# Optimization experiments

Hardware: AMD Instinct MI355X
Metric: run time of the kernel (lower is better)

The kernel has to match this reference:

```python
import jax, jax.numpy as jnp
import numpy as np

GROUP_SIZE = 128
ZERO_POINT = 8  # 4-bit symmetric zero point


def setup_inputs() -> dict:
    key = jax.random.key(0)
    k1, k2, k3, k4, k5, k6 = jax.random.split(key, 6)
    B, S, IN, OUT, RANK = 4, 2048, 4096, 4096, 32
    n_groups = IN // GROUP_SIZE  # 32
    x = jax.random.normal(k1, (B, S, IN), dtype=jnp.float32)
    q = jax.random.randint(k2, (OUT, IN), 0, 16, dtype=jnp.int32)  # 4-bit codes
    scales = jax.random.uniform(k3, (OUT, n_groups), dtype=jnp.float32)
    U = jax.random.normal(k4, (OUT, RANK), dtype=jnp.float32)
    V = jax.random.normal(k5, (RANK, IN), dtype=jnp.float32)
    bias = jax.random.normal(k6, (OUT,), dtype=jnp.float32)
    return {"x": x, "q": q, "scales": scales, "U": U, "V": V, "bias": bias}


def reference(x, q, scales, U, V, bias):
    out_f, in_f = q.shape
    n_groups = scales.shape[1]
    # Dequantize: per-group scaled 4-bit codes -> [out, in]
    qf = (q.astype(scales.dtype) - ZERO_POINT).reshape(out_f, n_groups, GROUP_SIZE)
    W = (qf * scales[:, :, None]).reshape(out_f, in_f)
    # Low-rank correction
    W = W + U @ V
    # F.linear: y = x @ W^T + b
    return jnp.einsum("bsi,oi->bso", x, W) + bias
```

## Files before the change

### kernel.cpp

```cpp
#include <hip/hip_runtime.h>
#include <hip/hip_bf16.h>

#define GAS __attribute__((address_space(1)))
#define LAS __attribute__((address_space(3)))

typedef __bf16 bf16x8 __attribute__((ext_vector_type(8)));
typedef float f32x16 __attribute__((ext_vector_type(16)));

constexpr int Kd = 4096;
constexpr int Nd = 4096;
constexpr int RANKd = 32;
constexpr int NG = 32;
constexpr int BM = 128, BN = 128, BK = 64;

constexpr int BWR = 32, BWC = 256;
constexpr int NBUILD = (Nd / BWR) * (Kd / BWC);

__global__ __launch_bounds__(256) void prep(
    const int* __restrict__ q, const float* __restrict__ scales,
    const float* __restrict__ U, const float* __restrict__ V,
    __hip_bfloat16* __restrict__ W,
    const float* __restrict__ x, __hip_bfloat16* __restrict__ xb)
{
  __shared__ float V_s[RANKd][BWC + 4];
  __shared__ float U_s[BWR][RANKd + 1];

  const int t = threadIdx.x;
  const int bid = blockIdx.x;

  if (bid >= NBUILD) {
    const size_t base = (size_t)(bid - NBUILD) * 8192;
    #pragma unroll
    for (int i = 0; i < 4; ++i) {
      const size_t idx = base + i * 2048 + t * 8;
      float4 a = *(const float4*)(x + idx);
      float4 b = *(const float4*)(x + idx + 4);
      union { __hip_bfloat16 h[8]; int4 v; } u;
      u.h[0] = __float2bfloat16(a.x); u.h[1] = __float2bfloat16(a.y);
      u.h[2] = __float2bfloat16(a.z); u.h[3] = __float2bfloat16(a.w);
      u.h[4] = __float2bfloat16(b.x); u.h[5] = __float2bfloat16(b.y);
      u.h[6] = __float2bfloat16(b.z); u.h[7] = __float2bfloat16(b.w);
      *(int4*)(xb + idx) = u.v;
    }
    return;
  }

  const int bx = bid & 15;
  const int by = bid >> 4;
  const int n0 = by * BWR;
  const int k0 = bx * BWC;

  {
    const int idx = t * 4;
    const int row = idx >> 5, rr = idx & 31;
    float4 uv = *(const float4*)(U + (size_t)(n0 + row) * RANKd + rr);
    U_s[row][rr] = uv.x; U_s[row][rr + 1] = uv.y;
    U_s[row][rr + 2] = uv.z; U_s[row][rr + 3] = uv.w;
  }
  #pragma unroll
  for (int i = 0; i < 8; ++i) {
    const int idx = i * 1024 + t * 4;
    const int vr = idx >> 8, vc = idx & 255;
    *(float4*)&V_s[vr][vc] = *(const float4*)(V + (size_t)vr * Kd + k0 + vc);
  }
  __syncthreads();

  const int rs = t >> 5;
  const int cs = t & 31;
  const int row0 = n0 + rs * 4;
  const int c0 = cs * 4;
  const int c1 = 128 + cs * 4;
  const int g0 = k0 >> 7, g1 = g0 + 1;

  float acc[4][8];
  #pragma unroll
  for (int j = 0; j < 4; ++j) {
    const int* qr = q + (size_t)(row0 + j) * Kd + k0;
    int4 a = *(const int4*)(qr + c0);
    int4 b = *(const int4*)(qr + c1);
    const float s0 = scales[(size_t)(row0 + j) * NG + g0];
    const float s1 = scales[(size_t)(row0 + j) * NG + g1];
    acc[j][0] = (float)(a.x - 8) * s0; acc[j][1] = (float)(a.y - 8) * s0;
    acc[j][2] = (float)(a.z - 8) * s0; acc[j][3] = (float)(a.w - 8) * s0;
    acc[j][4] = (float)(b.x - 8) * s1; acc[j][5] = (float)(b.y - 8) * s1;
    acc[j][6] = (float)(b.z - 8) * s1; acc[j][7] = (float)(b.w - 8) * s1;
  }

  #pragma unroll 4
  for (int r = 0; r < RANKd; ++r) {
    float4 v0 = *(const float4*)&V_s[r][c0];
    float4 v1 = *(const float4*)&V_s[r][c1];
    #pragma unroll
    for (int j = 0; j < 4; ++j) {
      const float u = U_s[rs * 4 + j][r];
      acc[j][0] += u * v0.x; acc[j][1] += u * v0.y;
      acc[j][2] += u * v0.z; acc[j][3] += u * v0.w;
      acc[j][4] += u * v1.x; acc[j][5] += u * v1.y;
      acc[j][6] += u * v1.z; acc[j][7] += u * v1.w;
    }
  }

  #pragma unroll
  for (int j = 0; j < 4; ++j) {
    union { __hip_bfloat16 h[4]; uint2 v; } o0, o1;
    o0.h[0] = __float2bfloat16(acc[j][0]); o0.h[1] = __float2bfloat16(acc[j][1]);
    o0.h[2] = __float2bfloat16(acc[j][2]); o0.h[3] = __float2bfloat16(acc[j][3]);
    o1.h[0] = __float2bfloat16(acc[j][4]); o1.h[1] = __float2bfloat16(acc[j][5]);
    o1.h[2] = __float2bfloat16(acc[j][6]); o1.h[3] = __float2bfloat16(acc[j][7]);
    __hip_bfloat16* wr = W + (size_t)(row0 + j) * Kd + k0;
    *(uint2*)(wr + c0) = o0.v;
    *(uint2*)(wr + c1) = o1.v;
  }
}

#define WAIT_VM6 asm volatile("s_waitcnt vmcnt(6)" ::: "memory")
#define WAIT_VM0 asm volatile("s_waitcnt vmcnt(0)" ::: "memory")
#define WAIT_NONE ((void)0)

#define ISSUE6(H, SLOT)                                                         \
  {                                                                             \
    char* sb_ = smc + (SLOT) * 24576;                                           \
    const size_t ko_ = (size_t)(H) * 32;                                        \
    __builtin_amdgcn_global_load_lds((GAS void*)(ag0 + ko_),                    \
        (LAS void*)(sb_ + ldsA), 16, 0, 0);                                     \
    __builtin_amdgcn_global_load_lds((GAS void*)(ag0 + 16 * Kd + ko_),          \
        (LAS void*)(sb_ + ldsA + 1024), 16, 0, 0);                              \
    __builtin_amdgcn_global_load_lds((GAS void*)(bg0 + ko_),                    \
        (LAS void*)(sb_ + ldsB), 16, 0, 0);                                     \
    __builtin_amdgcn_global_load_lds((GAS void*)(bg0 + 16 * Kd + ko_),          \
        (LAS void*)(sb_ + ldsB + 1024), 16, 0, 0);                              \
    __builtin_amdgcn_global_load_lds((GAS void*)(bg0 + 32 * Kd + ko_),          \
        (LAS void*)(sb_ + ldsB + 2048), 16, 0, 0);                              \
    __builtin_amdgcn_global_load_lds((GAS void*)(bg0 + 48 * Kd + ko_),          \
        (LAS void*)(sb_ + ldsB + 3072), 16, 0, 0);                              \
  }

#define GPHASE(G, SCUR, SNXT2, WAITSTMT, DO_ISSUE)                              \
  {                                                                             \
    const char* as_ = (const char*)smc + (SCUR) * 24576;                        \
    bf16x8 af0[4], af1[4], bfA[2], bfB[2];                                      \
    _Pragma("unroll")                                                           \
    for (int mi = 0; mi < 4; ++mi) {                                            \
      af0[mi] = *(const bf16x8*)(as_ + aro + mi * 2048 + cq0);                  \
      af1[mi] = *(const bf16x8*)(as_ + aro + mi * 2048 + cq1);                  \
    }                                                                           \
    _Pragma("unroll")                                                           \
    for (int nj = 0; nj < 2; ++nj) {                                            \
      bfA[nj] = *(const bf16x8*)(as_ + bro + nj * 2048 + cq0);                  \
      bfB[nj] = *(const bf16x8*)(as_ + bro + nj * 2048 + cq1);                  \
    }                                                                           \
    __builtin_amdgcn_sched_barrier(0);                                          \
    if (DO_ISSUE) { ISSUE6((G) + 2, SNXT2); }                                   \
    __builtin_amdgcn_sched_barrier(0);                                          \
    WAITSTMT;                                                                   \
    __builtin_amdgcn_s_barrier();                                               \
    asm volatile("s_waitcnt lgkmcnt(0)" ::: "memory");                          \
    __builtin_amdgcn_sched_barrier(0);                                          \
    __builtin_amdgcn_s_setprio(1);                                              \
    _Pragma("unroll")                                                           \
    for (int mi = 0; mi < 4; ++mi)                                              \
      _Pragma("unroll")                                                         \
      for (int nj = 0; nj < 2; ++nj)                                            \
        acc[mi][nj] = __builtin_amdgcn_mfma_f32_32x32x16_bf16(                  \
            af0[mi], bfA[nj], acc[mi][nj], 0, 0, 0);                            \
    _Pragma("unroll")                                                           \
    for (int mi = 0; mi < 4; ++mi)                                              \
      _Pragma("unroll")                                                         \
      for (int nj = 0; nj < 2; ++nj)                                            \
        acc[mi][nj] = __builtin_amdgcn_mfma_f32_32x32x16_bf16(                  \
            af1[mi], bfB[nj], acc[mi][nj], 0, 0, 0);                            \
    __builtin_amdgcn_s_setprio(0);                                              \
    __builtin_amdgcn_s_barrier();                                               \
  }

__global__ __launch_bounds__(256, 2) void gemm128(
    const __hip_bfloat16* __restrict__ A, const __hip_bfloat16* __restrict__ Bt,
    const float* __restrict__ bias, float* __restrict__ C)
{
  __shared__ __align__(16) char sm[73728];
  char* const smc = sm;

  int bx, by;
  {
    const int bid = blockIdx.x;
    if (gridDim.x == 1024) {
      const int x = bid & 7, loc = bid >> 3;
      by = x * 8 + (loc & 7);
      bx = loc >> 3;
    } else {
      by = bid >> 4;
      bx = bid & 15;
    }
  }
  const int bm0 = by * 128, bn0 = bx * 256;

  const int t = threadIdx.x;
  const int l = t & 63, w = t >> 6;

  const int sr   = l >> 2;
  const int schk = (l & 3) ^ ((l >> 3) & 3);
  const __hip_bfloat16* ag0 = A  + (size_t)(bm0 + w * 32 + sr) * Kd + schk * 8;
  const __hip_bfloat16* bg0 = Bt + (size_t)(bn0 + w * 64 + sr) * Kd + schk * 8;
  const int ldsA = w * 2048 + l * 16;
  const int ldsB = 8192 + w * 4096 + l * 16;

  const int rl = l & 31, kh = l >> 5, swz = (rl >> 1) & 3;
  const int aro = rl * 64;
  const int bro = 8192 + (w * 64 + rl) * 64;
  const int cq0 = (kh ^ swz) * 16;
  const int cq1 = ((2 + kh) ^ swz) * 16;

  f32x16 acc[4][2];
  #pragma unroll
  for (int mi = 0; mi < 4; ++mi)
    #pragma unroll
    for (int nj = 0; nj < 2; ++nj)
      acc[mi][nj] = (f32x16)(0.f);

  ISSUE6(0, 0);
  ISSUE6(1, 1);
  WAIT_VM6;
  __builtin_amdgcn_s_barrier();
  __builtin_amdgcn_sched_barrier(0);

  for (int g = 0; g < 126; g += 3) {
    GPHASE(g,     0, 2, WAIT_VM6, 1);
    GPHASE(g + 1, 1, 0, WAIT_VM6, 1);
    GPHASE(g + 2, 2, 1, WAIT_VM6, 1);
  }
  GPHASE(126, 0, 2, WAIT_VM0, 0);
  GPHASE(127, 1, 0, WAIT_NONE, 0);

  #pragma unroll
  for (int nj = 0; nj < 2; ++nj) {
    const int col = bn0 + w * 64 + nj * 32 + rl;
    const float bz = bias[col];
    #pragma unroll
    for (int mi = 0; mi < 4; ++mi) {
      const int rbase = bm0 + mi * 32 + 4 * kh;
      #pragma unroll
      for (int reg = 0; reg < 16; ++reg) {
        const int row = rbase + (reg & 3) + 8 * (reg >> 2);
        C[(size_t)row * Nd + col] = acc[mi][nj][reg] + bz;
      }
    }
  }
}

#undef GPHASE
#undef ISSUE6

template <bool ABF16>
__global__ __launch_bounds__(256) void gemm_bt(
    const void* __restrict__ Ap, const __hip_bfloat16* __restrict__ Bt,
    const float* __restrict__ bias, float* __restrict__ C)
{
  __shared__ __hip_bfloat16 As[BM * BK];
  __shared__ __hip_bfloat16 Bs[BN * BK];

  const int t  = threadIdx.x;
  const int l  = t & 63;
  const int w  = t >> 6;
  const int wm = w >> 1;
  const int wn = w & 1;
  const int bm0 = blockIdx.y * BM;
  const int bn0 = blockIdx.x * BN;

  f32x16 acc[2][2];
  #pragma unroll
  for (int i = 0; i < 2; ++i)
    #pragma unroll
    for (int j = 0; j < 2; ++j)
      acc[i][j] = (f32x16)(0.f);

  const __hip_bfloat16* Abf = (const __hip_bfloat16*)Ap;
  const float*          A32 = (const float*)Ap;

  const int sr   = l >> 2;
  const int schk = (l & 3) ^ ((l >> 3) & 3);
  const __hip_bfloat16* ag0 = Abf + (size_t)(bm0 + w * 32 + sr) * Kd + schk * 8;
  const __hip_bfloat16* bg0 = Bt  + (size_t)(bn0 + w * 32 + sr) * Kd + schk * 8;
  char* asb = (char*)As + w * 2048;
  char* bsb = (char*)Bs + w * 2048;

  const int rl = l & 31, kh = l >> 5, swz = (rl >> 1) & 3;
  const char* Ard = (const char*)As + (wm * 64 + rl) * 64;
  const char* Brd = (const char*)Bs + (wn * 64 + rl) * 64;

  const int arow = t >> 1, aslab = t & 1, arx = (arow >> 1) & 3;
  const float* a32p = A32 + (size_t)(bm0 + arow) * Kd + aslab * 32;
  char* awr = (char*)As + aslab * 8192 + arow * 64;

  for (int kt = 0; kt < Kd / BK; ++kt) {
    if constexpr (ABF16) {
      const __hip_bfloat16* ag = ag0 + kt * BK;
      __builtin_amdgcn_global_load_lds((GAS void*)ag,               (LAS void*)asb,                16, 0, 0);
      __builtin_amdgcn_global_load_lds((GAS void*)(ag + 16 * Kd),   (LAS void*)(asb + 1024),       16, 0, 0);
      __builtin_amdgcn_global_load_lds((GAS void*)(ag + 32),        (LAS void*)(asb + 8192),       16, 0, 0);
      __builtin_amdgcn_global_load_lds((GAS void*)(ag + 16*Kd + 32),(LAS void*)(asb + 8192 + 1024),16, 0, 0);
    } else {
      const float* ap = a32p + kt * BK;
      #pragma unroll
      for (int cc = 0; cc < 4; ++cc) {
        float4 f0 = ((const float4*)ap)[cc * 2];
        float4 f1 = ((const float4*)ap)[cc * 2 + 1];
        union { __hip_bfloat16 h[8]; int4 v; } u;
        u.h[0] = __float2bfloat16(f0.x); u.h[1] = __float2bfloat16(f0.y);
        u.h[2] = __float2bfloat16(f0.z); u.h[3] = __float2bfloat16(f0.w);
        u.h[4] = __float2bfloat16(f1.x); u.h[5] = __float2bfloat16(f1.y);
        u.h[6] = __float2bfloat16(f1.z); u.h[7] = __float2bfloat16(f1.w);
        *(int4*)(awr + ((cc ^ arx) * 16)) = u.v;
      }
    }
    {
      const __hip_bfloat16* bg = bg0 + kt * BK;
      __builtin_amdgcn_global_load_lds((GAS void*)bg,               (LAS void*)bsb,                16, 0, 0);
      __builtin_amdgcn_global_load_lds((GAS void*)(bg + 16 * Kd),   (LAS void*)(bsb + 1024),       16, 0, 0);
      __builtin_amdgcn_global_load_lds((GAS void*)(bg + 32),        (LAS void*)(bsb + 8192),       16, 0, 0);
      __builtin_amdgcn_global_load_lds((GAS void*)(bg + 16*Kd + 32),(LAS void*)(bsb + 8192 + 1024),16, 0, 0);
    }

    __syncthreads();

    bf16x8 af[2][4], bfr[2][4];
    #pragma unroll
    for (int mi = 0; mi < 2; ++mi)
      #pragma unroll
      for (int ks = 0; ks < 4; ++ks)
        af[mi][ks] = *(const bf16x8*)(Ard + (ks >> 1) * 8192 + mi * 2048 +
                                      ((((ks & 1) * 2 + kh) ^ swz) * 16));
    #pragma unroll
    for (int nj = 0; nj < 2; ++nj)
      #pragma unroll
      for (int ks = 0; ks < 4; ++ks)
        bfr[nj][ks] = *(const bf16x8*)(Brd + (ks >> 1) * 8192 + nj * 2048 +
                                       ((((ks & 1) * 2 + kh) ^ swz) * 16));

    #pragma unroll
    for (int ks = 0; ks < 4; ++ks)
      #pragma unroll
      for (int mi = 0; mi < 2; ++mi)
        #pragma unroll
        for (int nj = 0; nj < 2; ++nj)
          acc[mi][nj] = __builtin_amdgcn_mfma_f32_32x32x16_bf16(
              af[mi][ks], bfr[nj][ks], acc[mi][nj], 0, 0, 0);

    __syncthreads();
  }

  #pragma unroll
  for (int nj = 0; nj < 2; ++nj) {
    const int col = bn0 + wn * 64 + nj * 32 + rl;
    const float bz = bias[col];
    #pragma unroll
    for (int mi = 0; mi < 2; ++mi) {
      const int rbase = bm0 + wm * 64 + mi * 32 + 4 * kh;
      #pragma unroll
      for (int reg = 0; reg < 16; ++reg) {
        const int row = rbase + (reg & 3) + 8 * (reg >> 2);
        C[(size_t)row * Nd + col] = acc[mi][nj][reg] + bz;
      }
    }
  }
}

extern "C" void kernel_launch(void* const* d_in, const int* in_sizes, int n_in,
                              void* d_out, int out_size, void* d_ws, size_t ws_size,
                              hipStream_t stream)
{
  const float* x      = (const float*)d_in[0];
  const int*   q      = (const int*)  d_in[1];
  const float* scales = (const float*)d_in[2];
  const float* U      = (const float*)d_in[3];
  const float* V      = (const float*)d_in[4];
  const float* bias   = (const float*)d_in[5];
  float* out = (float*)d_out;

  const int M = in_sizes[0] / Kd;

  __hip_bfloat16* Wb = (__hip_bfloat16*)d_ws;
  const size_t wbytes = (size_t)Nd * Kd * sizeof(__hip_bfloat16);
  const size_t xbytes = (size_t)M  * Kd * sizeof(__hip_bfloat16);

  if (ws_size >= wbytes + xbytes && (M % 128) == 0) {
    __hip_bfloat16* Xb = (__hip_bfloat16*)((char*)d_ws + wbytes);
    const int nconv = (int)(((size_t)M * Kd) / 8192);
    prep<<<dim3(NBUILD + nconv), dim3(256), 0, stream>>>(q, scales, U, V, Wb, x, Xb);
    const int nblk = (M / 128) * (Nd / 256);
    gemm128<<<dim3(nblk), dim3(256), 0, stream>>>(Xb, Wb, bias, out);
  } else {
    prep<<<dim3(NBUILD), dim3(256), 0, stream>>>(q, scales, U, V, Wb, x, nullptr);
    dim3 grid(Nd / BN, M / BM);
    gemm_bt<false><<<grid, dim3(256), 0, stream>>>((const void*)x, Wb, bias, out);
  }
}
```

Before: 551.9 us.

## Load GEMM A fragments directly from global into registers, staging only B in LDS

The 128x256 GEMM now reads its A operand fragments straight from global memory into registers, one phase ahead. Only the B tile is staged in LDS through the triple-buffered async global-to-LDS path. This shrinks LDS use from 72 KB to 48 KB, drops the trailing barrier in each phase, and rebalances the vmcnt waits. The cost is that all four waves fetch the same A rows, so A traffic through the cache grows fourfold. The A loads also arrive in un-swizzled per-lane order, which may cause uncoalesced access and longer load latency in the MFMA loop.

After: 854.5 us. +54.8%, slower.

```diff
diff --git a/kernel.cpp b/kernel.cpp
--- a/kernel.cpp
+++ b/kernel.cpp
@@ -113,18 +113,14 @@
   }
 }
 
-#define WAIT_VM6 asm volatile("s_waitcnt vmcnt(6)" ::: "memory")
-#define WAIT_VM0 asm volatile("s_waitcnt vmcnt(0)" ::: "memory")
-#define WAIT_NONE ((void)0)
-
-#define ISSUE6(H, SLOT)                                                         \
+#define WAIT_VM12 asm volatile("s_waitcnt vmcnt(12)" ::: "memory")
+#define WAIT_VM4  asm volatile("s_waitcnt vmcnt(4)"  ::: "memory")
+#define WAIT_VM0  asm volatile("s_waitcnt vmcnt(0)"  ::: "memory")
+
+#define ISSUE_B(H, SLOT)                                                        \
   {                                                                             \
-    char* sb_ = smc + (SLOT) * 24576;                                           \
+    char* sb_ = smc + (SLOT) * 16384;                                           \
     const size_t ko_ = (size_t)(H) * 32;                                        \
-    __builtin_amdgcn_global_load_lds((GAS void*)(ag0 + ko_),                    \
-        (LAS void*)(sb_ + ldsA), 16, 0, 0);                                     \
-    __builtin_amdgcn_global_load_lds((GAS void*)(ag0 + 16 * Kd + ko_),          \
-        (LAS void*)(sb_ + ldsA + 1024), 16, 0, 0);                              \
     __builtin_amdgcn_global_load_lds((GAS void*)(bg0 + ko_),                    \
         (LAS void*)(sb_ + ldsB), 16, 0, 0);                                     \
     __builtin_amdgcn_global_load_lds((GAS void*)(bg0 + 16 * Kd + ko_),          \
@@ -135,26 +131,22 @@
         (LAS void*)(sb_ + ldsB + 3072), 16, 0, 0);                              \
   }
 
-#define GPHASE(G, SCUR, SNXT2, WAITSTMT, DO_ISSUE)                              \
+#define GPHASE(G, SCUR, SNXT2, WAITSTMT, DO_ISSUE, DO_AF)                       \
   {                                                                             \
-    const char* as_ = (const char*)smc + (SCUR) * 24576;                        \
-    bf16x8 af0[4], af1[4], bfA[2], bfB[2];                                      \
-    _Pragma("unroll")                                                           \
-    for (int mi = 0; mi < 4; ++mi) {                                            \
-      af0[mi] = *(const bf16x8*)(as_ + aro + mi * 2048 + cq0);                  \
-      af1[mi] = *(const bf16x8*)(as_ + aro + mi * 2048 + cq1);                  \
-    }                                                                           \
+    const char* bs_ = (const char*)smc + (SCUR) * 16384;                        \
+    bf16x8 bfA[2], bfB[2];                                                      \
     _Pragma("unroll")                                                           \
     for (int nj = 0; nj < 2; ++nj) {                                            \
-      bfA[nj] = *(const bf16x8*)(as_ + bro + nj * 2048 + cq0);                  \
-      bfB[nj] = *(const bf16x8*)(as_ + bro + nj * 2048 + cq1);                  \
+      bfA[nj] = *(const bf16x8*)(bs_ + bro + nj * 2048 + cq0);                  \
+      bfB[nj] = *(const bf16x8*)(bs_ + bro + nj * 2048 + cq1);                  \
     }                                                                           \
     __builtin_amdgcn_sched_barrier(0);                                          \
-    if (DO_ISSUE) { ISSUE6((G) + 2, SNXT2); }                                   \
+    if (DO_ISSUE) { ISSUE_B((G) + 2, SNXT2); }                                  \
     __builtin_amdgcn_sched_barrier(0);                                          \
     WAITSTMT;                                                                   \
+    asm volatile("s_waitcnt lgkmcnt(0)" ::: "memory");                          \
+    __builtin_amdgcn_sched_barrier(0);                                          \
     __builtin_amdgcn_s_barrier();                                               \
-    asm volatile("s_waitcnt lgkmcnt(0)" ::: "memory");                          \
     __builtin_amdgcn_sched_barrier(0);                                          \
     __builtin_amdgcn_s_setprio(1);                                              \
     _Pragma("unroll")                                                           \
@@ -170,14 +162,23 @@
         acc[mi][nj] = __builtin_amdgcn_mfma_f32_32x32x16_bf16(                  \
             af1[mi], bfB[nj], acc[mi][nj], 0, 0, 0);                            \
     __builtin_amdgcn_s_setprio(0);                                              \
-    __builtin_amdgcn_s_barrier();                                               \
+    __builtin_amdgcn_sched_barrier(0);                                          \
+    if (DO_AF) {                                                                \
+      _Pragma("unroll")                                                         \
+      for (int mi = 0; mi < 4; ++mi) {                                          \
+        af0[mi] = *(const bf16x8*)(aP[mi]);                                     \
+        af1[mi] = *(const bf16x8*)(aP[mi] + 32);                                \
+        aP[mi] += 64;                                                           \
+      }                                                                         \
+    }                                                                           \
+    __builtin_amdgcn_sched_barrier(0);                                          \
   }
 
 __global__ __launch_bounds__(256, 2) void gemm128(
     const __hip_bfloat16* __restrict__ A, const __hip_bfloat16* __restrict__ Bt,
     const float* __restrict__ bias, float* __restrict__ C)
 {
-  __shared__ __align__(16) char sm[73728];
+  __shared__ __align__(16) char sm[49152];
   char* const smc = sm;
 
   int bx, by;
@@ -199,17 +200,19 @@
 
   const int sr   = l >> 2;
   const int schk = (l & 3) ^ ((l >> 3) & 3);
-  const __hip_bfloat16* ag0 = A  + (size_t)(bm0 + w * 32 + sr) * Kd + schk * 8;
   const __hip_bfloat16* bg0 = Bt + (size_t)(bn0 + w * 64 + sr) * Kd + schk * 8;
-  const int ldsA = w * 2048 + l * 16;
-  const int ldsB = 8192 + w * 4096 + l * 16;
+  const int ldsB = w * 4096 + l * 16;
 
   const int rl = l & 31, kh = l >> 5, swz = (rl >> 1) & 3;
-  const int aro = rl * 64;
-  const int bro = 8192 + (w * 64 + rl) * 64;
+  const int bro = (w * 64 + rl) * 64;
   const int cq0 = (kh ^ swz) * 16;
   const int cq1 = ((2 + kh) ^ swz) * 16;
 
+  const char* aP[4];
+  #pragma unroll
+  for (int mi = 0; mi < 4; ++mi)
+    aP[mi] = (const char*)(A + (size_t)(bm0 + mi * 32 + rl) * Kd) + kh * 16;
+
   f32x16 acc[4][2];
   #pragma unroll
   for (int mi = 0; mi < 4; ++mi)
@@ -217,19 +220,29 @@
     for (int nj = 0; nj < 2; ++nj)
       acc[mi][nj] = (f32x16)(0.f);
 
-  ISSUE6(0, 0);
-  ISSUE6(1, 1);
-  WAIT_VM6;
+  bf16x8 af0[4], af1[4];
+
+  ISSUE_B(0, 0);
+  ISSUE_B(1, 1);
+  __builtin_amdgcn_sched_barrier(0);
+  #pragma unroll
+  for (int mi = 0; mi < 4; ++mi) {
+    af0[mi] = *(const bf16x8*)(aP[mi]);
+    af1[mi] = *(const bf16x8*)(aP[mi] + 32);
+    aP[mi] += 64;
+  }
+  __builtin_amdgcn_sched_barrier(0);
+  WAIT_VM12;
   __builtin_amdgcn_s_barrier();
   __builtin_amdgcn_sched_barrier(0);
 
   for (int g = 0; g < 126; g += 3) {
-    GPHASE(g,     0, 2, WAIT_VM6, 1);
-    GPHASE(g + 1, 1, 0, WAIT_VM6, 1);
-    GPHASE(g + 2, 2, 1, WAIT_VM6, 1);
-  }
-  GPHASE(126, 0, 2, WAIT_VM0, 0);
-  GPHASE(127, 1, 0, WAIT_NONE, 0);
+    GPHASE(g,     0, 2, WAIT_VM4, 1, 1);
+    GPHASE(g + 1, 1, 0, WAIT_VM4, 1, 1);
+    GPHASE(g + 2, 2, 1, WAIT_VM4, 1, 1);
+  }
+  GPHASE(126, 0, 2, WAIT_VM0, 0, 1);
+  GPHASE(127, 1, 0, WAIT_VM0, 0, 0);
 
   #pragma unroll
   for (int nj = 0; nj < 2; ++nj) {
@@ -248,7 +261,7 @@
 }
 
 #undef GPHASE
-#undef ISSUE6
+#undef ISSUE_B
 
 template <bool ABF16>
 __global__ __launch_bounds__(256) void gemm_bt(
```
